# Performance work log

Measured on AMD Instinct MI355X. Metric: run time of the kernel, lower is better.

## Reference

```python
import jax, jax.numpy as jnp
import numpy as np
from jax import lax

B, CIN, H, W = 16, 128, 56, 56
COUT, K, STRIDE, PAD, DIL = 256, 3, 1, 1, 1
D = 8  # lattice.d
KE = K * K
M = CIN * KE // D  # sub-vectors per spatial position


def setup_inputs() -> dict:
    key = jax.random.key(0)
    k1, k2, k3 = jax.random.split(key, 3)
    input_encodings = jax.random.normal(k1, (B, CIN, H, W), dtype=jnp.float32)
    weight_encodings = jax.random.normal(k2, (COUT, M, D), dtype=jnp.float32)
    bias = jax.random.normal(k3, (COUT,), dtype=jnp.float32)
    return {"input_encodings": input_encodings,
            "weight_encodings": weight_encodings,
            "bias": bias}


def reference(input_encodings, weight_encodings, bias):
    b, cin, h, w = input_encodings.shape
    cout, m, d = weight_encodings.shape
    h_out = (h + 2 * PAD - DIL * (K - 1) - 1) // STRIDE + 1
    w_out = (w + 2 * PAD - DIL * (K - 1) - 1) // STRIDE + 1
    L = h_out * w_out
    # im2col / unfold: (B, Cin*K*K, Hout, Wout), channel-major (c, kh, kw) ordering
    patches = lax.conv_general_dilated_patches(
        input_encodings, (K, K), (STRIDE, STRIDE), [(PAD, PAD), (PAD, PAD)],
        rhs_dilation=(DIL, DIL))
    # (B, L, M, D): each position split into M lattice-encoded sub-vectors of dim D
    x = patches.reshape(b, cin * K * K, L).transpose(0, 2, 1).reshape(b, L, m, d)
    # two-sided vLUT matrix multiply == sum of per-sub-vector inner products
    out = jnp.einsum('blmd,omd->bol', x, weight_encodings)  # (B, Cout, L)
    out = out.reshape(b, cout, h_out, w_out)
    return out + bias[None, :, None, None]
```

## Files before the change

### kernel.cpp

```cpp
#include <hip/hip_runtime.h>
#include <hip/hip_bf16.h>

#define CIN_   128
#define HW_    56
#define LHW_   3136
#define COUT_  256
#define KTOT_  1152
#define TH4_   4
#define SPB_   224
#define NF_    7
#define SCOLS_ 58
#define SPP4_  348
#define CSTR_  128

typedef unsigned short u16;
typedef __attribute__((ext_vector_type(8))) short short8v;
typedef __attribute__((ext_vector_type(4))) float f32x4;

__device__ __forceinline__ u16 f2bf(float f) {
  union { float f; unsigned u; } v; v.f = f;
  unsigned u = v.u;
  u += 0x7fffu + ((u >> 16) & 1u);
  return (u16)(u >> 16);
}
__device__ __forceinline__ unsigned pack2(u16 a, u16 b) {
  return (unsigned)a | ((unsigned)b << 16);
}

__global__ void wreorder2_kernel(const float* __restrict__ w, u16* __restrict__ wb,
                                 u16* __restrict__ zp) {
  if (blockIdx.x == 0 && threadIdx.x < 16) {
    uint4 z; z.x = z.y = z.z = z.w = 0u;
    reinterpret_cast<uint4*>(zp)[threadIdx.x] = z;
  }
  int j = blockIdx.x * 256 + threadIdx.x;
  int c4 = j & 31;
  int o  = (j >> 5) & 255;
  int t  = j >> 13;
  int c0i = c4 >> 3;
  int lg  = (c4 >> 1) & 3;
  size_t slot = ((size_t)(t * 4 + c0i) * 16 + (o >> 4)) * 64 + lg * 16 + (o & 15);
  const float* src = w + (size_t)o * KTOT_ + t;
  ushort4 r;
  r.x = f2bf(src[(c4 * 4 + 0) * 9]);
  r.y = f2bf(src[(c4 * 4 + 1) * 9]);
  r.z = f2bf(src[(c4 * 4 + 2) * 9]);
  r.w = f2bf(src[(c4 * 4 + 3) * 9]);
  *reinterpret_cast<ushort4*>(wb + slot * 8 + (c4 & 1) * 4) = r;
}

__global__ void wreorder_kernel(const float* __restrict__ w, u16* __restrict__ wb) {
  int j = blockIdx.x * 256 + threadIdx.x;
  int c4 = j & 31;
  int o  = (j >> 5) & 255;
  int t  = j >> 13;
  const float* src = w + (size_t)o * KTOT_ + t;
  ushort4 r;
  r.x = f2bf(src[(c4 * 4 + 0) * 9]);
  r.y = f2bf(src[(c4 * 4 + 1) * 9]);
  r.z = f2bf(src[(c4 * 4 + 2) * 9]);
  r.w = f2bf(src[(c4 * 4 + 3) * 9]);
  *reinterpret_cast<ushort4*>(wb + ((size_t)(t * 256 + o) * CSTR_ + c4 * 4)) = r;
}

#define TLDSW_ 136
__global__ __launch_bounds__(256) void nhwc_kernel(
    const float* __restrict__ in, u16* __restrict__ xin) {
  __shared__ u16 ts[64 * TLDSW_];
  const int bp = blockIdx.x;
  const int b = bp / 49;
  const int pos0 = (bp % 49) * 64;
  const int tid = threadIdx.x;
  const float* ib = in + (size_t)b * CIN_ * LHW_ + pos0;
  {
    const int p  = tid & 63;
    const int c0 = (tid >> 6) * 32;
    #pragma unroll
    for (int i = 0; i < 32; ++i)
      ts[p * TLDSW_ + c0 + i] = f2bf(ib[(size_t)(c0 + i) * LHW_ + p]);
  }
  __syncthreads();
  {
    const int p  = tid >> 2;
    const int c0 = (tid & 3) * 32;
    u16* dst = xin + ((size_t)b * LHW_ + pos0 + p) * CIN_ + c0;
    const u16* srcr = &ts[p * TLDSW_ + c0];
    #pragma unroll
    for (int j = 0; j < 4; ++j)
      reinterpret_cast<uint4*>(dst)[j] =
          *reinterpret_cast<const uint4*>(srcr + j * 8);
  }
}

__device__ __forceinline__ void gload_lds16(const void* g, void* l) {
  __builtin_amdgcn_global_load_lds(
      (const __attribute__((address_space(1))) void*)g,
      (__attribute__((address_space(3))) void*)l, 16, 0, 0);
}

__global__ __launch_bounds__(512, 2) void conv4_kernel(
    const u16* __restrict__ xin, const u16* __restrict__ wb2,
    const float* __restrict__ bias, const u16* __restrict__ zpage,
    float* __restrict__ out)
{
  __shared__ u16 xs[SPP4_ * CSTR_];

  const int tid  = threadIdx.x;
  const int lane = tid & 63;
  const int wid  = tid >> 6;
  const int wc   = wid & 3;
  const int ws   = wid >> 2;
  const int lr   = lane & 15;
  const int lg   = lane >> 4;
  const int lg8  = lg * 8;

  const int ty = blockIdx.x % 14;
  const int b  = blockIdx.x / 14;
  const int iy0 = ty * TH4_ - 1;

  const u16* xb = xin + (size_t)b * LHW_ * CIN_;

  #pragma unroll
  for (int i = 0; i < 11; ++i) {
    int idx = i * 512 + tid;
    if (idx < SPP4_ * 16) {
      int spp   = idx >> 4;
      int chunk = idx & 15;
      int rr = spp / SCOLS_;
      int cc = spp - rr * SCOLS_;
      int iy = iy0 + rr;
      int ix = cc - 1;
      int sch = chunk ^ (spp & 7);
      const u16* src =
          ((unsigned)iy < (unsigned)HW_ && (unsigned)ix < (unsigned)HW_)
              ? xb + ((size_t)(iy * HW_ + ix) * CIN_ + sch * 8)
              : zpage;
      u16* ldst = xs + (size_t)(idx & ~63) * 8;
      gload_lds16(src, ldst);
    }
  }

  int spp0[NF_];
  #pragma unroll
  for (int nf = 0; nf < NF_; ++nf) {
    int sp = ws * 112 + nf * 16 + lr;
    int r  = sp / 56;
    int x  = sp - r * 56;
    spp0[nf] = (r + 1) * SCOLS_ + (x + 1);
  }

  f32x4 acc[4][NF_];
  #pragma unroll
  for (int m = 0; m < 4; ++m)
    #pragma unroll
    for (int nf = 0; nf < NF_; ++nf)
      acc[m][nf] = f32x4{0.f, 0.f, 0.f, 0.f};

  __syncthreads();

  const short8v* pA = reinterpret_cast<const short8v*>(wb2);

  auto loadA = [&](int t4c, short8v* dst) {
    const short8v* p = pA + ((size_t)t4c * 16 + wc * 4) * 64 + lane;
    #pragma unroll
    for (int ai = 0; ai < 4; ++ai) dst[ai] = p[ai * 64];
  };
  auto loadB = [&](int dspp, int c0, short8v* dst) {
    #pragma unroll
    for (int nf = 0; nf < NF_; ++nf) {
      int spp = spp0[nf] + dspp;
      int off = (spp << 7) + ((c0 + lg8) ^ ((spp & 7) << 3));
      dst[nf] = *reinterpret_cast<const short8v*>(&xs[off]);
    }
  };

  short8v A0[4], A1[4], B0[NF_], B1[NF_];

#define MFMA_GRP(Ab, Bb)                                                        \
  {                                                                             \
    _Pragma("unroll")                                                           \
    for (int ai = 0; ai < 4; ++ai) {                                            \
      _Pragma("unroll")                                                         \
      for (int nf = 0; nf < NF_; ++nf)                                          \
        acc[ai][nf] = __builtin_amdgcn_mfma_f32_16x16x32_bf16(                  \
            (Ab)[ai], (Bb)[nf], acc[ai][nf], 0, 0, 0);                          \
    }                                                                           \
  }

  loadA(0, A0);
  loadB(-SCOLS_ - 1, 0, B0);

  #pragma unroll 1
  for (int t = 0; t < 9; ++t) {
    const int dty  = t / 3;
    const int dspp = (dty - 1) * SCOLS_ + (t - 3 * dty) - 1;
    const int t4   = t * 4;

    loadA(t4 + 1, A1); loadB(dspp, 32, B1);
    MFMA_GRP(A0, B0);
    loadA(t4 + 2, A0); loadB(dspp, 64, B0);
    MFMA_GRP(A1, B1);
    loadA(t4 + 3, A1); loadB(dspp, 96, B1);
    MFMA_GRP(A0, B0);
    if (t < 8) {
      const int tn   = t + 1;
      const int ndty = tn / 3;
      const int nds  = (ndty - 1) * SCOLS_ + (tn - 3 * ndty) - 1;
      loadA(t4 + 4, A0); loadB(nds, 0, B0);
    }
    MFMA_GRP(A1, B1);
  }

  float* ob = out + (size_t)b * COUT_ * LHW_ + ty * SPB_ + ws * 112;
  const int obase = wc * 64 + lg * 4;
  #pragma unroll
  for (int ai = 0; ai < 4; ++ai) {
    #pragma unroll
    for (int rr = 0; rr < 4; ++rr) {
      const int o = obase + ai * 16 + rr;
      const float bs = bias[o];
      #pragma unroll
      for (int nf = 0; nf < NF_; ++nf)
        ob[(size_t)o * LHW_ + nf * 16 + lr] = acc[ai][nf][rr] + bs;
    }
  }
#undef MFMA_GRP
}

#define TH_    2
#define SPT_   112
#define SPP_   232
__global__ __launch_bounds__(256, 2) void conv2_kernel(
    const float* __restrict__ in, const u16* __restrict__ wb,
    const float* __restrict__ bias, float* __restrict__ out)
{
  __shared__ u16 xs[SPP_ * CSTR_];
  const int tid  = threadIdx.x;
  const int lane = tid & 63;
  const int wid  = tid >> 6;
  const int lr   = lane & 15;
  const int lg   = lane >> 4;
  const int bid = blockIdx.x;
  const int ch  = bid & 1;
  const int ty  = (bid >> 1) % 28;
  const int b   = bid / 56;
  const float* inb = in + (size_t)b * CIN_ * LHW_;
  const int iy0 = ty * TH_ - 1;

  #pragma unroll 1
  for (int i = 0; i < 15; ++i) {
    int idx = i * 256 + tid;
    if (idx < SPP_ * 16) {
      int cg  = idx / SPP_;
      int spp = idx - cg * SPP_;
      int rr  = spp / SCOLS_;
      int cc  = spp - rr * SCOLS_;
      int iy  = iy0 + rr;
      int ix  = cc - 1;
      bool ok = ((unsigned)iy < (unsigned)HW_) && ((unsigned)ix < (unsigned)HW_);
      const float* p = inb + (size_t)cg * 8 * LHW_ + iy * HW_ + ix;
      u16 v[8];
      #pragma unroll
      for (int jj = 0; jj < 8; ++jj)
        v[jj] = f2bf(ok ? p[jj * LHW_] : 0.f);
      uint4 pk;
      pk.x = pack2(v[0], v[1]); pk.y = pack2(v[2], v[3]);
      pk.z = pack2(v[4], v[5]); pk.w = pack2(v[6], v[7]);
      *reinterpret_cast<uint4*>(&xs[spp * CSTR_ + ((cg * 8) ^ ((spp & 7) << 3))]) = pk;
    }
  }
  int spp0[NF_];
  #pragma unroll
  for (int nf = 0; nf < NF_; ++nf) {
    int sp = nf * 16 + lr;
    int r  = (sp >= 56) ? 1 : 0;
    int x  = sp - r * 56;
    spp0[nf] = (r + 1) * SCOLS_ + x + 1;
  }
  f32x4 acc[2][NF_];
  #pragma unroll
  for (int m = 0; m < 2; ++m)
    #pragma unroll
    for (int nf = 0; nf < NF_; ++nf)
      acc[m][nf] = f32x4{0.f, 0.f, 0.f, 0.f};
  __syncthreads();
  const u16* wt0 = wb + (size_t)(ch * 128 + wid * 32 + lr) * CSTR_ + lg * 8;
  #pragma unroll 1
  for (int t = 0; t < 9; ++t) {
    const int dspp = (t / 3 - 1) * SCOLS_ + (t % 3 - 1);
    const u16* wt = wt0 + (size_t)t * 256 * CSTR_;
    #pragma unroll
    for (int c0i = 0; c0i < 4; ++c0i) {
      const int c0 = c0i * 32;
      short8v a0 = *reinterpret_cast<const short8v*>(wt + c0);
      short8v a1 = *reinterpret_cast<const short8v*>(wt + 16 * CSTR_ + c0);
      short8v bv[NF_];
      #pragma unroll
      for (int nf = 0; nf < NF_; ++nf) {
        int spp = spp0[nf] + dspp;
        int off = spp * CSTR_ + ((c0 + lg * 8) ^ ((spp & 7) << 3));
        bv[nf] = *reinterpret_cast<const short8v*>(&xs[off]);
      }
      #pragma unroll
      for (int nf = 0; nf < NF_; ++nf) {
        acc[0][nf] = __builtin_amdgcn_mfma_f32_16x16x32_bf16(a0, bv[nf], acc[0][nf], 0, 0, 0);
        acc[1][nf] = __builtin_amdgcn_mfma_f32_16x16x32_bf16(a1, bv[nf], acc[1][nf], 0, 0, 0);
      }
    }
  }
  float* ob = out + (size_t)b * COUT_ * LHW_ + ty * SPT_;
  const int obase = ch * 128 + wid * 32 + lg * 4;
  #pragma unroll
  for (int m = 0; m < 2; ++m)
    #pragma unroll
    for (int rr = 0; rr < 4; ++rr) {
      const int o = obase + m * 16 + rr;
      const float bs = bias[o];
      #pragma unroll
      for (int nf = 0; nf < NF_; ++nf)
        ob[(size_t)o * LHW_ + nf * 16 + lr] = acc[m][nf][rr] + bs;
    }
}

#define SPT0_  64
#define BK0_   32
#define NKS0_  36
#define LDSW0_ 40
__global__ __launch_bounds__(256, 2) void conv_fb_kernel(
    const float* __restrict__ in, const float* __restrict__ wf,
    const float* __restrict__ bias, float* __restrict__ out)
{
  __shared__ u16 xs[SPT0_ * LDSW0_];
  const int tid = threadIdx.x;
  const int lane = tid & 63;
  const int wid = tid >> 6;
  const int lg = lane >> 4;
  const int lr = lane & 15;
  const int bid = blockIdx.x;
  const int b = bid / 49;
  const int l0 = (bid % 49) * SPT0_;
  const int sp = tid & 63;
  const int qq = tid >> 6;
  const int l = l0 + sp;
  const int y = l / HW_;
  const int x = l - y * HW_;
  const float* inb = in + (size_t)b * CIN_ * LHW_;
  f32x4 acc[4][4];
  #pragma unroll
  for (int i = 0; i < 4; ++i)
    #pragma unroll
    for (int j = 0; j < 4; ++j) acc[i][j] = f32x4{0.f, 0.f, 0.f, 0.f};
  auto stage_load = [&](int ks) -> uint4 {
    int kbase = ks * BK0_ + qq * 8;
    int c = kbase / 9;
    int t = kbase - c * 9;
    u16 v[8];
    #pragma unroll
    for (int j = 0; j < 8; ++j) {
      int dy = (t * 11) >> 5;
      int dx = t - 3 * dy;
      int yy = y + dy - 1, xx = x + dx - 1;
      float f = 0.f;
      if ((unsigned)yy < (unsigned)HW_ && (unsigned)xx < (unsigned)HW_)
        f = inb[(c * HW_ + yy) * HW_ + xx];
      v[j] = f2bf(f);
      ++t; if (t == 9) { t = 0; ++c; }
    }
    uint4 r;
    r.x = pack2(v[0], v[1]); r.y = pack2(v[2], v[3]);
    r.z = pack2(v[4], v[5]); r.w = pack2(v[6], v[7]);
    return r;
  };
  uint4 st = stage_load(0);
  for (int ks = 0; ks < NKS0_; ++ks) {
    __syncthreads();
    *reinterpret_cast<uint4*>(&xs[sp * LDSW0_ + qq * 8]) = st;
    __syncthreads();
    if (ks + 1 < NKS0_) st = stage_load(ks + 1);
    const int k0 = ks * BK0_;
    short8v a[4];
    #pragma unroll
    for (int ai = 0; ai < 4; ++ai) {
      const int o = wid * 64 + ai * 16 + lr;
      const float* p = wf + (size_t)o * KTOT_ + k0 + lg * 8;
      u16 t8[8];
      #pragma unroll
      for (int j = 0; j < 8; ++j) t8[j] = f2bf(p[j]);
      union { uint4 u; short8v s; } cv;
      cv.u.x = pack2(t8[0], t8[1]); cv.u.y = pack2(t8[2], t8[3]);
      cv.u.z = pack2(t8[4], t8[5]); cv.u.w = pack2(t8[6], t8[7]);
      a[ai] = cv.s;
    }
    short8v bv[4];
    #pragma unroll
    for (int sj = 0; sj < 4; ++sj)
      bv[sj] = *reinterpret_cast<const short8v*>(&xs[(sj * 16 + lr) * LDSW0_ + lg * 8]);
    #pragma unroll
    for (int ai = 0; ai < 4; ++ai)
      #pragma unroll
      for (int sj = 0; sj < 4; ++sj)
        acc[ai][sj] = __builtin_amdgcn_mfma_f32_16x16x32_bf16(a[ai], bv[sj], acc[ai][sj], 0, 0, 0);
  }
  float* outb = out + (size_t)b * COUT_ * LHW_ + l0;
  #pragma unroll
  for (int ai = 0; ai < 4; ++ai)
    #pragma unroll
    for (int r = 0; r < 4; ++r) {
      const int o = wid * 64 + ai * 16 + lg * 4 + r;
      const float bvs = bias[o];
      #pragma unroll
      for (int sj = 0; sj < 4; ++sj)
        outb[(size_t)o * LHW_ + sj * 16 + lr] = acc[ai][sj][r] + bvs;
    }
}

extern "C" void kernel_launch(void* const* d_in, const int* in_sizes, int n_in,
                              void* d_out, int out_size, void* d_ws, size_t ws_size,
                              hipStream_t stream) {
  (void)in_sizes; (void)n_in; (void)out_size;
  const float* in   = (const float*)d_in[0];
  const float* w    = (const float*)d_in[1];
  const float* bias = (const float*)d_in[2];
  float* out = (float*)d_out;

  const size_t wbytes  = (size_t)COUT_ * KTOT_ * sizeof(u16);
  const size_t xbytes  = (size_t)16 * LHW_ * CIN_ * sizeof(u16);
  const size_t need    = wbytes + xbytes + 256;

  if (ws_size >= need) {
    u16* wb2 = (u16*)d_ws;
    u16* xin = wb2 + wbytes / 2;
    u16* zp  = xin + xbytes / 2;
    wreorder2_kernel<<<dim3(288), dim3(256), 0, stream>>>(w, wb2, zp);
    nhwc_kernel<<<dim3(784), dim3(256), 0, stream>>>(in, xin);
    conv4_kernel<<<dim3(224), dim3(512), 0, stream>>>(xin, wb2, bias, zp, out);
  } else if (ws_size >= wbytes) {
    u16* wb = (u16*)d_ws;
    wreorder_kernel<<<dim3(288), dim3(256), 0, stream>>>(w, wb);
    conv2_kernel<<<dim3(896), dim3(256), 0, stream>>>(in, wb, bias, out);
  } else {
    conv_fb_kernel<<<dim3(784), dim3(256), 0, stream>>>(in, w, bias, out);
  }
}
```

Before: 61.77 us.

## Shrink conv tile to two rows per block, swizzle block order, prioritize MFMA

Replaces the 512-thread, four-row conv4 kernel with a 256-thread, two-row conv5 kernel launched as 448 blocks, so more blocks are spread across the 256 CUs and the work is less lopsided per CU. Block indices are swizzled across batches to change L2 locality. MFMA groups are wrapped in s_setprio so the matrix work gets issue priority over loads. The cost is more halo rows loaded per output row (232 vs 348 for double the rows) and more weight reloads per output.

Measured after the change: 67.27 us. 8.9% more time.

```diff
diff --git a/kernel.cpp b/kernel.cpp
--- a/kernel.cpp
+++ b/kernel.cpp
@@ -6,11 +6,11 @@
 #define LHW_   3136
 #define COUT_  256
 #define KTOT_  1152
-#define TH4_   4
-#define SPB_   224
+#define TH_    2
+#define SPT_   112
 #define NF_    7
 #define SCOLS_ 58
-#define SPP4_  348
+#define SPP_   232
 #define CSTR_  128
 
 typedef unsigned short u16;
@@ -98,32 +98,31 @@
       (__attribute__((address_space(3))) void*)l, 16, 0, 0);
 }
 
-__global__ __launch_bounds__(512, 2) void conv4_kernel(
+__global__ __launch_bounds__(256, 2) void conv5_kernel(
     const u16* __restrict__ xin, const u16* __restrict__ wb2,
     const float* __restrict__ bias, const u16* __restrict__ zpage,
     float* __restrict__ out)
 {
-  __shared__ u16 xs[SPP4_ * CSTR_];
+  __shared__ u16 xs[SPP_ * CSTR_];
 
   const int tid  = threadIdx.x;
   const int lane = tid & 63;
-  const int wid  = tid >> 6;
-  const int wc   = wid & 3;
-  const int ws   = wid >> 2;
+  const int wc   = tid >> 6;
   const int lr   = lane & 15;
   const int lg   = lane >> 4;
   const int lg8  = lg * 8;
 
-  const int ty = blockIdx.x % 14;
-  const int b  = blockIdx.x / 14;
-  const int iy0 = ty * TH4_ - 1;
+  const int swz = (blockIdx.x & 7) * 56 + (blockIdx.x >> 3);
+  const int b   = swz / 28;
+  const int ty  = swz % 28;
+  const int iy0 = ty * TH_ - 1;
 
   const u16* xb = xin + (size_t)b * LHW_ * CIN_;
 
   #pragma unroll
-  for (int i = 0; i < 11; ++i) {
-    int idx = i * 512 + tid;
-    if (idx < SPP4_ * 16) {
+  for (int i = 0; i < 15; ++i) {
+    int idx = i * 256 + tid;
+    if (idx < SPP_ * 16) {
       int spp   = idx >> 4;
       int chunk = idx & 15;
       int rr = spp / SCOLS_;
@@ -143,8 +142,8 @@
   int spp0[NF_];
   #pragma unroll
   for (int nf = 0; nf < NF_; ++nf) {
-    int sp = ws * 112 + nf * 16 + lr;
-    int r  = sp / 56;
+    int sp = nf * 16 + lr;
+    int r  = (sp >= 56) ? 1 : 0;
     int x  = sp - r * 56;
     spp0[nf] = (r + 1) * SCOLS_ + (x + 1);
   }
@@ -178,6 +177,7 @@
 
 #define MFMA_GRP(Ab, Bb)                                                        \
   {                                                                             \
+    __builtin_amdgcn_s_setprio(1);                                              \
     _Pragma("unroll")                                                           \
     for (int ai = 0; ai < 4; ++ai) {                                            \
       _Pragma("unroll")                                                         \
@@ -185,6 +185,7 @@
         acc[ai][nf] = __builtin_amdgcn_mfma_f32_16x16x32_bf16(                  \
             (Ab)[ai], (Bb)[nf], acc[ai][nf], 0, 0, 0);                          \
     }                                                                           \
+    __builtin_amdgcn_s_setprio(0);                                              \
   }
 
   loadA(0, A0);
@@ -211,7 +212,7 @@
     MFMA_GRP(A1, B1);
   }
 
-  float* ob = out + (size_t)b * COUT_ * LHW_ + ty * SPB_ + ws * 112;
+  float* ob = out + (size_t)b * COUT_ * LHW_ + ty * SPT_;
   const int obase = wc * 64 + lg * 4;
   #pragma unroll
   for (int ai = 0; ai < 4; ++ai) {
@@ -227,9 +228,6 @@
 #undef MFMA_GRP
 }
 
-#define TH_    2
-#define SPT_   112
-#define SPP_   232
 __global__ __launch_bounds__(256, 2) void conv2_kernel(
     const float* __restrict__ in, const u16* __restrict__ wb,
     const float* __restrict__ bias, float* __restrict__ out)
@@ -433,7 +431,7 @@
     u16* zp  = xin + xbytes / 2;
     wreorder2_kernel<<<dim3(288), dim3(256), 0, stream>>>(w, wb2, zp);
     nhwc_kernel<<<dim3(784), dim3(256), 0, stream>>>(in, xin);
-    conv4_kernel<<<dim3(224), dim3(512), 0, stream>>>(xin, wb2, bias, zp, out);
+    conv5_kernel<<<dim3(448), dim3(256), 0, stream>>>(xin, wb2, bias, zp, out);
   } else if (ws_size >= wbytes) {
     u16* wb = (u16*)d_ws;
     wreorder_kernel<<<dim3(288), dim3(256), 0, stream>>>(w, wb);
```
